# Optimization experiments

Hardware: AMD Instinct MI355X
Metric: run time of the kernel (lower is better)

## Reference

```python
import jax, jax.numpy as jnp
import numpy as np


def setup_inputs() -> dict:
    key = jax.random.key(0)
    k = jax.random.split(key, 6)
    B = 65536
    return {
        "x": jax.random.normal(k[0], (B, 784), dtype=jnp.float32),
        "conv_w": jax.random.normal(k[1], (3, 3), dtype=jnp.float32),
        "fc1_w": jax.random.normal(k[2], (128, 676), dtype=jnp.float32) * 0.04,
        "fc1_b": jax.random.normal(k[3], (128,), dtype=jnp.float32),
        "fc2_w": jax.random.normal(k[4], (10, 128), dtype=jnp.float32) * 0.09,
        "fc2_b": jax.random.normal(k[5], (10,), dtype=jnp.float32),
    }


def reference(x, conv_w, fc1_w, fc1_b, fc2_w, fc2_b):
    B = x.shape[0]
    img = x.reshape(B, 1, 28, 28)  # NCHW, single channel
    # Valid cross-correlation with a 3x3 kernel (matches the torch sum(region*weight) loop)
    kern = conv_w.reshape(1, 1, 3, 3)  # OIHW
    conv = jax.lax.conv_general_dilated(
        img, kern, window_strides=(1, 1), padding="VALID",
        dimension_numbers=("NCHW", "OIHW", "NCHW"))  # [B,1,26,26]
    h = conv.reshape(B, 26 * 26)
    h = jax.nn.relu(h @ fc1_w.T + fc1_b)  # [B,128]
    logits = h @ fc2_w.T + fc2_b  # [B,10]
    return logits
```

## Files before the change

kernel.cpp:

```cpp
#include <hip/hip_runtime.h>

typedef __bf16 bf16x8 __attribute__((ext_vector_type(8)));
typedef float  f32x4  __attribute__((ext_vector_type(4)));

#define KDIM    784
#define KSTEP   32
#define NSTEPS  25
#define NCOLS   128
#define NT      8
#define WAVES   4
#define ROWS_PER_WAVE 32
#define ROWS_PER_BLOCK (WAVES * ROWS_PER_WAVE)
#define XSTEP_BYTES 16384
#define WSTEP_BYTES 8192
#define HSH_PAD 132
#define HCHUNK  16

__global__ __launch_bounds__(64) void prep_weff(
    const float* __restrict__ conv_w,
    const float* __restrict__ fc1_w,
    __bf16* __restrict__ wfrag)
{
  int idx = blockIdx.x * 64 + threadIdx.x;
  if (idx >= NSTEPS * NT * 64) return;
  int lane = idx & 63;
  int n    = (idx >> 6) & (NT - 1);
  int s    = idx >> 9;
  int col  = n * 16 + (lane & 15);
  int kb   = s * KSTEP + (lane >> 4) * 8;
  bf16x8 o;
#pragma unroll
  for (int j = 0; j < 8; ++j) {
    int k = kb + j;
    float v = 0.f;
    if (k < KDIM) {
      int r = k / 28, c = k % 28;
#pragma unroll
      for (int u = 0; u < 3; ++u)
#pragma unroll
        for (int w = 0; w < 3; ++w) {
          int p = r - u, q = c - w;
          if (p >= 0 && p < 26 && q >= 0 && q < 26)
            v = fmaf(conv_w[u * 3 + w], fc1_w[col * 676 + p * 26 + q], v);
        }
    }
    o[j] = (__bf16)v;
  }
  reinterpret_cast<bf16x8*>(wfrag)[idx] = o;
}

__device__ __forceinline__ bf16x8 pack8(f32x4 lo, f32x4 hi) {
  bf16x8 r;
  r[0] = (__bf16)lo[0]; r[1] = (__bf16)lo[1];
  r[2] = (__bf16)lo[2]; r[3] = (__bf16)lo[3];
  r[4] = (__bf16)hi[0]; r[5] = (__bf16)hi[1];
  r[6] = (__bf16)hi[2]; r[7] = (__bf16)hi[3];
  return r;
}

__device__ __forceinline__ void split8(f32x4 a, f32x4 b, bf16x8& hi, bf16x8& lo) {
#pragma unroll
  for (int j = 0; j < 4; ++j) {
    __bf16 h = (__bf16)a[j]; hi[j] = h; lo[j] = (__bf16)(a[j] - (float)h);
  }
#pragma unroll
  for (int j = 0; j < 4; ++j) {
    __bf16 h = (__bf16)b[j]; hi[4 + j] = h; lo[4 + j] = (__bf16)(b[j] - (float)h);
  }
}

__device__ __forceinline__ void stage_copy(
    const float* __restrict__ xrowbase, const __bf16* __restrict__ wfrag,
    unsigned char* smem, int buf, int t, int wave, int lane)
{
  unsigned char* xdst = smem + buf * XSTEP_BYTES;
  int sb = ((lane & 7) * 16) ^ (((lane >> 3) & 7) << 4);
  int row_off = t * 128 + sb;
  if (row_off + 16 > KDIM * 4) row_off = 0;
#pragma unroll
  for (int i = 0; i < 4; ++i) {
    int c = wave * 4 + i;
    const unsigned char* src =
        (const unsigned char*)(xrowbase + (size_t)(c * 8 + (lane >> 3)) * KDIM) + row_off;
    unsigned char* dst = xdst + c * 1024 + lane * 16;
    __builtin_amdgcn_global_load_lds(
        (const __attribute__((address_space(1))) unsigned int*)src,
        (__attribute__((address_space(3))) unsigned int*)dst, 16, 0, 0);
  }
  unsigned char* wdst = smem + 2 * XSTEP_BYTES + buf * WSTEP_BYTES;
  const unsigned char* wsrc = (const unsigned char*)wfrag + (size_t)t * WSTEP_BYTES;
#pragma unroll
  for (int i = 0; i < 2; ++i) {
    int c = wave * 2 + i;
    const unsigned char* src = wsrc + c * 1024 + lane * 16;
    unsigned char* dst = wdst + c * 1024 + lane * 16;
    __builtin_amdgcn_global_load_lds(
        (const __attribute__((address_space(1))) unsigned int*)src,
        (__attribute__((address_space(3))) unsigned int*)dst, 16, 0, 0);
  }
}

__global__ __launch_bounds__(256, 2) void fused_mlp(
    const float*  __restrict__ x,
    const __bf16* __restrict__ wfrag,
    const float*  __restrict__ fc1_b,
    const float*  __restrict__ fc2_w,
    const float*  __restrict__ fc2_b,
    float*        __restrict__ out)
{
  __shared__ __align__(16) unsigned char smem[2 * XSTEP_BYTES + 2 * WSTEP_BYTES];
  float (*hsh)[HCHUNK][HSH_PAD] =
      reinterpret_cast<float (*)[HCHUNK][HSH_PAD]>(smem);

  int tid  = threadIdx.x;
  int wave = tid >> 6, lane = tid & 63;
  int lrow = lane & 15;
  int lgrp = lane >> 4;
  long wrow0 = (long)blockIdx.x * ROWS_PER_BLOCK + wave * ROWS_PER_WAVE;
  const float* xrowbase = x + (long)blockIdx.x * ROWS_PER_BLOCK * KDIM;

  f32x4 acc[2][NT];
#pragma unroll
  for (int m = 0; m < 2; ++m)
#pragma unroll
    for (int n = 0; n < NT; ++n) acc[m][n] = (f32x4){0.f, 0.f, 0.f, 0.f};

  int base0 = (wave * 32 + lrow) * 128;
  int base1 = base0 + 16 * 128;
  int swz   = (lrow & 7) << 4;
  int sb0   = (lgrp * 32) ^ swz;
  int sb1   = (lgrp * 32 + 16) ^ swz;

  stage_copy(xrowbase, wfrag, smem, 0, 0, wave, lane);

  for (int t = 0; t < NSTEPS; ++t) {
    __syncthreads();
    if (t < NSTEPS - 1)
      stage_copy(xrowbase, wfrag, smem, (t + 1) & 1, t + 1, wave, lane);

    int buf = t & 1;
    const unsigned char* xb = smem + buf * XSTEP_BYTES;
    const bf16x8* bp =
        (const bf16x8*)(smem + 2 * XSTEP_BYTES + buf * WSTEP_BYTES) + lane;

    f32x4 x00 = *(const f32x4*)(xb + base0 + sb0);
    f32x4 x01 = *(const f32x4*)(xb + base0 + sb1);
    f32x4 x10 = *(const f32x4*)(xb + base1 + sb0);
    f32x4 x11 = *(const f32x4*)(xb + base1 + sb1);
    bf16x8 a0 = pack8(x00, x01);
    bf16x8 a1 = pack8(x10, x11);

    bf16x8 bf[NT];
#pragma unroll
    for (int n = 0; n < NT; ++n) bf[n] = bp[n * 64];
#pragma unroll
    for (int n = 0; n < NT; ++n) {
      acc[0][n] = __builtin_amdgcn_mfma_f32_16x16x32_bf16(a0, bf[n], acc[0][n], 0, 0, 0);
      acc[1][n] = __builtin_amdgcn_mfma_f32_16x16x32_bf16(a1, bf[n], acc[1][n], 0, 0, 0);
    }
  }
  __syncthreads();

  int osafe = (lrow < 10) ? lrow : 9;
  bf16x8 whi[4], wlo[4];
#pragma unroll
  for (int s2 = 0; s2 < 4; ++s2) {
    f32x4 w0 = *(const f32x4*)(fc2_w + osafe * NCOLS + s2 * 32 + lgrp * 8);
    f32x4 w1 = *(const f32x4*)(fc2_w + osafe * NCOLS + s2 * 32 + lgrp * 8 + 4);
    if (lrow >= 10) { w0 = (f32x4){0.f,0.f,0.f,0.f}; w1 = (f32x4){0.f,0.f,0.f,0.f}; }
    split8(w0, w1, whi[s2], wlo[s2]);
  }
  float b2 = (lrow < 10) ? fc2_b[lrow] : 0.f;
  float bcol[NT];
#pragma unroll
  for (int n = 0; n < NT; ++n) bcol[n] = fc1_b[n * 16 + lrow];

#pragma unroll
  for (int m2 = 0; m2 < 2; ++m2) {
#pragma unroll
    for (int n = 0; n < NT; ++n) {
      int col = n * 16 + lrow;
#pragma unroll
      for (int ri = 0; ri < 4; ++ri) {
        int rl = lgrp * 4 + ri;
        hsh[wave][rl][col] = fmaxf(acc[m2][n][ri] + bcol[n], 0.f);
      }
    }
    f32x4 acc2 = (f32x4){0.f, 0.f, 0.f, 0.f};
    const float* hr = &hsh[wave][lrow][0];
#pragma unroll
    for (int s2 = 0; s2 < 4; ++s2) {
      f32x4 h0 = *(const f32x4*)(hr + s2 * 32 + lgrp * 8);
      f32x4 h1 = *(const f32x4*)(hr + s2 * 32 + lgrp * 8 + 4);
      bf16x8 ahi, alo; split8(h0, h1, ahi, alo);
      acc2 = __builtin_amdgcn_mfma_f32_16x16x32_bf16(ahi, whi[s2], acc2, 0, 0, 0);
      acc2 = __builtin_amdgcn_mfma_f32_16x16x32_bf16(ahi, wlo[s2], acc2, 0, 0, 0);
      acc2 = __builtin_amdgcn_mfma_f32_16x16x32_bf16(alo, whi[s2], acc2, 0, 0, 0);
    }
    if (lrow < 10) {
#pragma unroll
      for (int ri = 0; ri < 4; ++ri)
        out[(wrow0 + m2 * 16 + lgrp * 4 + ri) * 10 + lrow] = acc2[ri] + b2;
    }
  }
}

extern "C" void kernel_launch(void* const* d_in, const int* in_sizes, int n_in,
                              void* d_out, int out_size, void* d_ws, size_t ws_size,
                              hipStream_t stream) {
  const float* x      = (const float*)d_in[0];
  const float* conv_w = (const float*)d_in[1];
  const float* fc1_w  = (const float*)d_in[2];
  const float* fc1_b  = (const float*)d_in[3];
  const float* fc2_w  = (const float*)d_in[4];
  const float* fc2_b  = (const float*)d_in[5];
  float* outp = (float*)d_out;
  __bf16* wfrag = (__bf16*)d_ws;

  int Btotal = in_sizes[0] / KDIM;
  int prep_threads = NSTEPS * NT * 64;

  hipLaunchKernelGGL(prep_weff, dim3(prep_threads / 64), dim3(64), 0, stream,
                     conv_w, fc1_w, wfrag);
  hipLaunchKernelGGL(fused_mlp, dim3(Btotal / ROWS_PER_BLOCK), dim3(256), 0, stream,
                     x, wfrag, fc1_b, fc2_w, fc2_b, outp);
}
```

Measured before the change: 46.99 us.

## Triple-buffer LDS staging with two-step prefetch and explicit vmcnt waits

Switches the K-loop from double to triple buffering in LDS, so global-to-LDS copies for step t+2 are issued while step t is being computed. The full __syncthreads is replaced with a partial s_waitcnt vmcnt(6) plus s_barrier, which lets the newest copies stay in flight. This is meant to hide more global load latency. In exchange LDS use per block grows from 48KB to 72KB, which may cut how many blocks fit on each CU.

```diff
diff --git a/kernel.cpp b/kernel.cpp
--- a/kernel.cpp
+++ b/kernel.cpp
@@ -13,6 +13,7 @@
 #define ROWS_PER_BLOCK (WAVES * ROWS_PER_WAVE)
 #define XSTEP_BYTES 16384
 #define WSTEP_BYTES 8192
+#define NBUF 3
 #define HSH_PAD 132
 #define HCHUNK  16
 
@@ -87,7 +88,7 @@
         (const __attribute__((address_space(1))) unsigned int*)src,
         (__attribute__((address_space(3))) unsigned int*)dst, 16, 0, 0);
   }
-  unsigned char* wdst = smem + 2 * XSTEP_BYTES + buf * WSTEP_BYTES;
+  unsigned char* wdst = smem + NBUF * XSTEP_BYTES + buf * WSTEP_BYTES;
   const unsigned char* wsrc = (const unsigned char*)wfrag + (size_t)t * WSTEP_BYTES;
 #pragma unroll
   for (int i = 0; i < 2; ++i) {
@@ -108,7 +109,7 @@
     const float*  __restrict__ fc2_b,
     float*        __restrict__ out)
 {
-  __shared__ __align__(16) unsigned char smem[2 * XSTEP_BYTES + 2 * WSTEP_BYTES];
+  __shared__ __align__(16) unsigned char smem[NBUF * XSTEP_BYTES + NBUF * WSTEP_BYTES];
   float (*hsh)[HCHUNK][HSH_PAD] =
       reinterpret_cast<float (*)[HCHUNK][HSH_PAD]>(smem);
 
@@ -131,34 +132,50 @@
   int sb0   = (lgrp * 32) ^ swz;
   int sb1   = (lgrp * 32 + 16) ^ swz;
 
+#define STEP_COMPUTE(BUF)                                                      \
+  {                                                                            \
+    const unsigned char* xb = smem + (BUF) * XSTEP_BYTES;                      \
+    const bf16x8* bp =                                                         \
+        (const bf16x8*)(smem + NBUF * XSTEP_BYTES + (BUF) * WSTEP_BYTES) + lane; \
+    f32x4 x00 = *(const f32x4*)(xb + base0 + sb0);                             \
+    f32x4 x01 = *(const f32x4*)(xb + base0 + sb1);                             \
+    f32x4 x10 = *(const f32x4*)(xb + base1 + sb0);                             \
+    f32x4 x11 = *(const f32x4*)(xb + base1 + sb1);                             \
+    bf16x8 a0 = pack8(x00, x01);                                               \
+    bf16x8 a1 = pack8(x10, x11);                                               \
+    bf16x8 bf[NT];                                                             \
+    _Pragma("unroll")                                                          \
+    for (int n = 0; n < NT; ++n) bf[n] = bp[n * 64];                           \
+    _Pragma("unroll")                                                          \
+    for (int n = 0; n < NT; ++n) {                                             \
+      acc[0][n] = __builtin_amdgcn_mfma_f32_16x16x32_bf16(a0, bf[n], acc[0][n], 0, 0, 0); \
+      acc[1][n] = __builtin_amdgcn_mfma_f32_16x16x32_bf16(a1, bf[n], acc[1][n], 0, 0, 0); \
+    }                                                                          \
+  }
+
   stage_copy(xrowbase, wfrag, smem, 0, 0, wave, lane);
-
-  for (int t = 0; t < NSTEPS; ++t) {
-    __syncthreads();
-    if (t < NSTEPS - 1)
-      stage_copy(xrowbase, wfrag, smem, (t + 1) & 1, t + 1, wave, lane);
-
-    int buf = t & 1;
-    const unsigned char* xb = smem + buf * XSTEP_BYTES;
-    const bf16x8* bp =
-        (const bf16x8*)(smem + 2 * XSTEP_BYTES + buf * WSTEP_BYTES) + lane;
-
-    f32x4 x00 = *(const f32x4*)(xb + base0 + sb0);
-    f32x4 x01 = *(const f32x4*)(xb + base0 + sb1);
-    f32x4 x10 = *(const f32x4*)(xb + base1 + sb0);
-    f32x4 x11 = *(const f32x4*)(xb + base1 + sb1);
-    bf16x8 a0 = pack8(x00, x01);
-    bf16x8 a1 = pack8(x10, x11);
-
-    bf16x8 bf[NT];
-#pragma unroll
-    for (int n = 0; n < NT; ++n) bf[n] = bp[n * 64];
-#pragma unroll
-    for (int n = 0; n < NT; ++n) {
-      acc[0][n] = __builtin_amdgcn_mfma_f32_16x16x32_bf16(a0, bf[n], acc[0][n], 0, 0, 0);
-      acc[1][n] = __builtin_amdgcn_mfma_f32_16x16x32_bf16(a1, bf[n], acc[1][n], 0, 0, 0);
-    }
-  }
+  stage_copy(xrowbase, wfrag, smem, 1, 1, wave, lane);
+  __builtin_amdgcn_sched_barrier(0);
+  asm volatile("s_waitcnt vmcnt(6)" ::: "memory");
+  __builtin_amdgcn_s_barrier();
+
+  int cur = 0;
+  for (int t = 0; t < NSTEPS - 2; ++t) {
+    int iss = cur + 2; if (iss >= NBUF) iss -= NBUF;
+    stage_copy(xrowbase, wfrag, smem, iss, t + 2, wave, lane);
+    STEP_COMPUTE(cur);
+    __builtin_amdgcn_sched_barrier(0);
+    asm volatile("s_waitcnt vmcnt(6)" ::: "memory");
+    __builtin_amdgcn_s_barrier();
+    ++cur; if (cur >= NBUF) cur -= NBUF;
+  }
+
+  STEP_COMPUTE(cur);
+  asm volatile("s_waitcnt vmcnt(0)" ::: "memory");
+  __builtin_amdgcn_s_barrier();
+  ++cur; if (cur >= NBUF) cur -= NBUF;
+
+  STEP_COMPUTE(cur);
   __syncthreads();
 
   int osafe = (lrow < 10) ? lrow : 9;
```

Result: no change. 47.57 us (+1.2%).
